# Performance work log

Hardware: AMD Instinct MI355X
Metric: run time of the kernel (lower is better)

## Reference

```python
import jax, jax.numpy as jnp
import numpy as np

RADIUS = 8
NUM_CORNERS = 500


def _dwconv(x, k2d, mode):
    # depthwise 2D conv on NCHW with explicit border padding (kornia-style)
    ph, pw = k2d.shape[0] // 2, k2d.shape[1] // 2
    xp = jnp.pad(x, ((0, 0), (0, 0), (ph, ph), (pw, pw)), mode=mode)
    C = x.shape[1]
    kern = jnp.broadcast_to(k2d[None, None], (C, 1, k2d.shape[0], k2d.shape[1])).astype(x.dtype)
    return jax.lax.conv_general_dilated(xp, kern, (1, 1), 'VALID',
                                        feature_group_count=C,
                                        dimension_numbers=('NCHW', 'OIHW', 'NCHW'))


def _gauss2d(k, sigma):
    x = jnp.arange(k, dtype=jnp.float32) - (k - 1) / 2.0
    g = jnp.exp(-(x * x) / (2.0 * sigma * sigma))
    g = g / g.sum()
    return jnp.outer(g, g)


def _nms2d(x):
    # kornia.feature.nms2d with (5,5) window: keep values equal to local max
    m = jax.lax.reduce_window(x, -jnp.inf, jax.lax.max, (1, 1, 5, 5), (1, 1, 1, 1), 'SAME')
    return x * (x == m).astype(x.dtype)


def _gftt(gray):
    # kornia CornerGFTT: sobel gradients (normalized /8, replicate pad),
    # structure tensor blurred with gaussian(7, sigma=1), min eigenvalue
    kx = jnp.array([[-1., 0., 1.], [-2., 0., 2.], [-1., 0., 1.]], jnp.float32) / 8.0
    dx = _dwconv(gray, kx, 'edge')
    dy = _dwconv(gray, kx.T, 'edge')
    g7 = _gauss2d(7, 1.0)
    dx2 = _dwconv(dx * dx, g7, 'reflect')
    dy2 = _dwconv(dy * dy, g7, 'reflect')
    dxy = _dwconv(dx * dy, g7, 'reflect')
    det = dx2 * dy2 - dxy * dxy
    tr = dx2 + dy2
    return 0.5 * (tr - jnp.sqrt(jnp.abs(tr * tr - 4.0 * det)))


def _laplacian5(x):
    # kornia laplacian kernel size 5, normalized by abs-sum (=48), reflect pad
    k = jnp.ones((5, 5), jnp.float32).at[2, 2].set(1.0 - 25.0)
    k = k / jnp.abs(k).sum()
    return _dwconv(x, k, 'reflect')


def _get_corners(imgs):
    B, _, H, W = imgs.shape
    r, N = RADIUS, NUM_CORNERS
    gray = 0.299 * imgs[:, :1] + 0.587 * imgs[:, 1:2] + 0.114 * imgs[:, 2:3]
    corners = _nms2d(_gftt(gray))
    # MaxPool2d(r, return_indices) + MaxUnpool2d(r): keep only per-block max
    blocks = corners.reshape(B, 1, H // r, r, W // r, r)
    bmax = blocks.max(axis=(3, 5), keepdims=True)
    unpooled = jnp.where(blocks == bmax, blocks, 0.0).reshape(B, 1, H, W)
    values, idx = jax.lax.top_k(unpooled.reshape(B, -1), N)   # [B,N]
    h, w = idx // W, idx % W
    b = jnp.repeat(jnp.arange(B), N)
    target = jnp.zeros((B, 1, H, W), imgs.dtype).at[b, 0, h.ravel(), w.ravel()].set(values.ravel())
    target = _nms2d(target)
    return (target > 0).astype(target.dtype)


def setup_inputs() -> dict:
    key = jax.random.key(0)
    k1, k2 = jax.random.split(key)
    scores_dense = jax.random.uniform(k1, (16, 1, 512, 512), dtype=jnp.float32)
    imgs = jax.random.uniform(k2, (16, 3, 512, 512), dtype=jnp.float32)
    return {"scores_dense": scores_dense, "imgs": imgs}


def reference(scores_dense, imgs):
    corners = _dwconv(_get_corners(imgs), _gauss2d(7, 1.0), 'reflect')
    lap = _laplacian5(scores_dense)
    logp = jnp.clip(jnp.log(scores_dense), -100.0)      # torch BCELoss clamps log at -100
    log1mp = jnp.clip(jnp.log1p(-scores_dense), -100.0)
    bce = -(corners * logp + (1.0 - corners) * log1mp).mean()
    return bce + (scores_dense * jnp.exp(-lap)).mean() * 10.0
```

## Files before the change

### kernel.cpp

```cpp
#include <hip/hip_runtime.h>
#include <math.h>

#define BB 16
#define HH 512
#define WW 512
#define HWP (HH*WW)
#define NPIX (BB*HWP)
#define HWP4 (HWP/4)
#define NG (NPIX/4)
#define NCORN 500
#define NSLOT 4096
#define OCAP 1024
#define NKEY (NSLOT+OCAP)
#define NKPT (NKEY/256)
#define NBL 2048
#define NPOSTB 320

__device__ __constant__ float G7c[7] = {
    0.0044330482f, 0.0540055826f, 0.2420362294f, 0.3990502793f,
    0.2420362294f, 0.0540055826f, 0.0044330482f};

__device__ __forceinline__ int reflect_idx(int i, int n) {
    if (i < 0) i = -i;
    if (i >= n) i = 2 * n - 2 - i;
    return i;
}

__device__ __forceinline__ float w1d(int p, int o, int n) {
    float w = 0.f;
    int d = p - o;
    if (d >= -3 && d <= 3) w += G7c[d + 3];
    if (p >= 1 && p + o <= 3) w += G7c[3 - p - o];
    if (p <= n - 2 && p + o >= 2 * n - 5) w += G7c[2 * n + 1 - p - o];
    return w;
}

__global__ void k_gray(const float* __restrict__ imgs, float* __restrict__ gray) {
    int g = blockIdx.x * blockDim.x + threadIdx.x;
    if (g >= NG) return;
    int b = g / HWP4, r = g % HWP4;
    const float4* base = (const float4*)(imgs + (size_t)b * 3 * HWP);
    float4 R = base[r], G = base[r + HWP4], Bc = base[r + 2 * HWP4];
    float4 o;
    o.x = 0.299f * R.x + 0.587f * G.x + 0.114f * Bc.x;
    o.y = 0.299f * R.y + 0.587f * G.y + 0.114f * Bc.y;
    o.z = 0.299f * R.z + 0.587f * G.z + 0.114f * Bc.z;
    o.w = 0.299f * R.w + 0.587f * G.w + 0.114f * Bc.w;
    ((float4*)gray)[g] = o;
}

__global__ __launch_bounds__(256) void k_front(const float* __restrict__ gray,
                                               float* __restrict__ S) {
    __shared__ float gt[24][72];
    __shared__ float pA[22][70], pC[22][70], pD[22][70];
    __shared__ float hA[22][64], hC[22][64], hD[22][64];
    int x0 = blockIdx.x * 64;
    int y0 = blockIdx.y * 16;
    int b = blockIdx.z;
    const float* gb = gray + (size_t)b * HWP;
    int tid = threadIdx.x;

    for (int idx = tid; idx < 24 * 72; idx += 256) {
        int r = idx / 72, c = idx % 72;
        int gy = min(max(y0 - 4 + r, 0), HH - 1);
        int gx = min(max(x0 - 4 + c, 0), WW - 1);
        gt[r][c] = gb[gy * WW + gx];
    }
    __syncthreads();

    for (int idx = tid; idx < 22 * 70; idx += 256) {
        int r = idx / 70, c = idx % 70;
        int py = y0 - 3 + r, px = x0 - 3 + c;
        if (py >= 0 && py < HH && px >= 0 && px < WW) {
            float g00 = gt[r][c],   g01 = gt[r][c+1],   g02 = gt[r][c+2];
            float g10 = gt[r+1][c],                     g12 = gt[r+1][c+2];
            float g20 = gt[r+2][c], g21 = gt[r+2][c+1], g22 = gt[r+2][c+2];
            float dx = (g02 - g00 + 2.f * (g12 - g10) + g22 - g20) * 0.125f;
            float dy = (g20 - g00 + 2.f * (g21 - g01) + g22 - g02) * 0.125f;
            pA[r][c] = dx * dx; pC[r][c] = dy * dy; pD[r][c] = dx * dy;
        }
    }
    __syncthreads();

    for (int idx = tid; idx < 22 * 64; idx += 256) {
        int r = idx / 64, c = idx % 64;
        int py = y0 - 3 + r;
        if (py >= 0 && py < HH) {
            int ox = x0 + c;
            float A = 0.f, C = 0.f, D = 0.f;
#pragma unroll
            for (int t = 0; t < 7; ++t) {
                int px = reflect_idx(ox - 3 + t, WW);
                int lc = px - (x0 - 3);
                float w = G7c[t];
                A += w * pA[r][lc]; C += w * pC[r][lc]; D += w * pD[r][lc];
            }
            hA[r][c] = A; hC[r][c] = C; hD[r][c] = D;
        }
    }
    __syncthreads();

    for (int idx = tid; idx < 16 * 64; idx += 256) {
        int r = idx / 64, c = idx % 64;
        int oy = y0 + r;
        float A = 0.f, C = 0.f, D = 0.f;
#pragma unroll
        for (int t = 0; t < 7; ++t) {
            int py = reflect_idx(oy - 3 + t, HH);
            int lr = py - (y0 - 3);
            float w = G7c[t];
            A += w * hA[lr][c]; C += w * hC[lr][c]; D += w * hD[lr][c];
        }
        float det = A * C - D * D;
        float tr = A + C;
        S[(size_t)b * HWP + (size_t)oy * WW + x0 + c] =
            0.5f * (tr - sqrtf(fabsf(tr * tr - 4.f * det)));
    }
}

__global__ void k_cand2(const float* __restrict__ S, float* __restrict__ sval,
                        int* __restrict__ sidx, int* __restrict__ ocnt) {
    __shared__ float tile[4][12][12];
    int wave = threadIdx.x >> 6, lane = threadIdx.x & 63;
    int tx = blockIdx.x * 4 + wave;
    int ty = blockIdx.y;
    int b = blockIdx.z;
    const float* sb = S + (size_t)b * HWP;
    for (int t = lane; t < 144; t += 64) {
        int r = t / 12, c = t % 12;
        int yy = min(max(ty * 8 - 2 + r, 0), HH - 1);
        int xx = min(max(tx * 8 - 2 + c, 0), WW - 1);
        tile[wave][r][c] = sb[yy * WW + xx];
    }
    __syncthreads();
    int ly = lane >> 3, lx = lane & 7;
    float v = tile[wave][ly + 2][lx + 2];
    float m = -INFINITY;
#pragma unroll
    for (int dy = 0; dy < 5; ++dy)
#pragma unroll
        for (int dx = 0; dx < 5; ++dx)
            m = fmaxf(m, tile[wave][ly + dy][lx + dx]);
    float cval = (v == m) ? v : 0.f;
    int y = ty * 8 + ly, x = tx * 8 + lx;
    float tm = cval;
#pragma unroll
    for (int off = 32; off; off >>= 1)
        tm = fmaxf(tm, __shfl_xor(tm, off));
    unsigned long long mask = __ballot(cval == tm && cval > 0.f);
    int slot = ty * 64 + tx;
    if (mask) {
        int first = __ffsll(mask) - 1;
        if (lane == first) {
            sval[b * NKEY + slot] = cval;
            sidx[b * NKEY + slot] = y * WW + x;
        } else if ((mask >> lane) & 1ull) {
            int pos = atomicAdd(&ocnt[b], 1);
            if (pos < OCAP) {
                sval[b * NKEY + NSLOT + pos] = cval;
                sidx[b * NKEY + NSLOT + pos] = y * WW + x;
            }
        }
    } else if (lane == 0) {
        sval[b * NKEY + slot] = 0.f;
        sidx[b * NKEY + slot] = 0;
    }
}

__global__ __launch_bounds__(256) void k_sel(const float* __restrict__ sval,
                       const int* __restrict__ sidx, const int* __restrict__ ocnt,
                       unsigned long long* __restrict__ selK) {
    __shared__ int shw[4];
    __shared__ int shtot;
    int b = blockIdx.x;
    int n = NSLOT + min(ocnt[b], OCAP);
    unsigned long long keys[NKPT];
    int cnt = 0;
#pragma unroll
    for (int t = 0; t < NKPT; ++t) {
        int i = threadIdx.x + t * 256;
        unsigned long long k = 0ull;
        if (i < n) {
            float v = sval[b * NKEY + i];
            if (v > 0.f) {
                unsigned int ix = (unsigned int)sidx[b * NKEY + i];
                k = ((unsigned long long)__float_as_uint(v) << 32) |
                    (unsigned long long)(~ix);
                cnt++;
            }
        }
        keys[t] = k;
    }
    int wid = threadIdx.x >> 6;
    {
        int c = cnt;
#pragma unroll
        for (int off = 32; off; off >>= 1) c += __shfl_down(c, off);
        if ((threadIdx.x & 63) == 0) shw[wid] = c;
        __syncthreads();
        if (threadIdx.x == 0) shtot = shw[0] + shw[1] + shw[2] + shw[3];
        __syncthreads();
    }
    int target = min(NCORN, shtot);
    unsigned long long T = 0ull;
    for (int bit = 63; bit >= 0; --bit) {
        unsigned long long cand = T | (1ull << bit);
        int c = 0;
#pragma unroll
        for (int t = 0; t < NKPT; ++t) c += (keys[t] >= cand) ? 1 : 0;
#pragma unroll
        for (int off = 32; off; off >>= 1) c += __shfl_down(c, off);
        __syncthreads();
        if ((threadIdx.x & 63) == 0) shw[wid] = c;
        __syncthreads();
        int tot = shw[0] + shw[1] + shw[2] + shw[3];
        if (tot >= target) T = cand;
    }
    if (threadIdx.x == 0) selK[b] = T;
}

__global__ __launch_bounds__(256) void k_post(const float* __restrict__ sval,
                       const int* __restrict__ sidx, const int* __restrict__ ocnt,
                       const unsigned long long* __restrict__ selK,
                       const float* __restrict__ scores,
                       float* __restrict__ partialC) {
    int gid = blockIdx.x * 256 + threadIdx.x;
    int b = gid / NKEY, s = gid - b * NKEY;
    int novf = min(ocnt[b], OCAP);
    float contrib = 0.f;
    float v = (s < NSLOT + novf) ? sval[gid] : 0.f;
    if (v > 0.f) {
        unsigned int ix = (unsigned int)sidx[gid];
        unsigned long long K = selK[b];
        unsigned long long k = ((unsigned long long)__float_as_uint(v) << 32) |
                               (unsigned long long)(~ix);
        if (k >= K) {
            int y = (int)(ix >> 9), x = (int)(ix & 511);
            const float* bsv = sval + b * NKEY;
            const int* bsi = sidx + b * NKEY;
            bool sup = false;
            int ty0 = max(y - 2, 0) >> 3, ty1 = min(y + 2, HH - 1) >> 3;
            int tx0 = max(x - 2, 0) >> 3, tx1 = min(x + 2, WW - 1) >> 3;
            for (int ty = ty0; ty <= ty1 && !sup; ++ty)
                for (int tx = tx0; tx <= tx1 && !sup; ++tx) {
                    int s2 = ty * 64 + tx;
                    float v2 = bsv[s2];
                    if (v2 <= v) continue;
                    int ix2 = bsi[s2];
                    unsigned long long k2 = ((unsigned long long)__float_as_uint(v2) << 32) |
                                            (unsigned long long)(~(unsigned int)ix2);
                    if (k2 < K) continue;
                    int y2 = ix2 >> 9, x2 = ix2 & 511;
                    if (abs(y2 - y) <= 2 && abs(x2 - x) <= 2) sup = true;
                }
            for (int j = 0; j < novf && !sup; ++j) {
                float v2 = bsv[NSLOT + j];
                if (v2 <= v) continue;
                int ix2 = bsi[NSLOT + j];
                unsigned long long k2 = ((unsigned long long)__float_as_uint(v2) << 32) |
                                        (unsigned long long)(~(unsigned int)ix2);
                if (k2 < K) continue;
                int y2 = ix2 >> 9, x2 = ix2 & 511;
                if (abs(y2 - y) <= 2 && abs(x2 - x) <= 2) sup = true;
            }
            if (!sup) {
                const float* sb = scores + (size_t)b * HWP;
                if (y >= 3 && y <= HH - 4 && x >= 3 && x <= WW - 4) {
#pragma unroll
                    for (int j = -3; j <= 3; ++j) {
                        float wy = G7c[j + 3];
#pragma unroll
                        for (int i = -3; i <= 3; ++i) {
                            float w = wy * G7c[i + 3];
                            float p = sb[(y + j) * WW + (x + i)];
                            float lp = fmaxf(__logf(p), -100.f);
                            float l1p = fmaxf(__logf(1.f - p), -100.f);
                            contrib += w * (lp - l1p);
                        }
                    }
                } else {
                    int oy0 = max(y - 6, 0), oy1 = min(y + 6, HH - 1);
                    int ox0 = max(x - 6, 0), ox1 = min(x + 6, WW - 1);
                    for (int oy = oy0; oy <= oy1; ++oy) {
                        float wy = w1d(y, oy, HH);
                        if (wy == 0.f) continue;
                        for (int ox = ox0; ox <= ox1; ++ox) {
                            float wx = w1d(x, ox, WW);
                            if (wx == 0.f) continue;
                            float p = sb[oy * WW + ox];
                            float lp = fmaxf(__logf(p), -100.f);
                            float l1p = fmaxf(__logf(1.f - p), -100.f);
                            contrib += wy * wx * (lp - l1p);
                        }
                    }
                }
            }
        }
    }
#pragma unroll
    for (int off = 32; off; off >>= 1) contrib += __shfl_down(contrib, off);
    __shared__ float wsum[4];
    int wid = threadIdx.x >> 6;
    if ((threadIdx.x & 63) == 0) wsum[wid] = contrib;
    __syncthreads();
    if (threadIdx.x == 0)
        partialC[blockIdx.x] = wsum[0] + wsum[1] + wsum[2] + wsum[3];
}

__global__ __launch_bounds__(256) void k_loss(const float* __restrict__ scores,
                                              float* __restrict__ partial) {
    __shared__ float st[8][520];
    __shared__ float h5[8][512];
    int b = blockIdx.x >> 7;
    int rg = blockIdx.x & 127;
    int y0 = rg * 4;
    const float* sb = scores + (size_t)b * HWP;
    int tid = threadIdx.x;
    for (int idx = tid; idx < 8 * 516; idx += 256) {
        int i = idx / 516, c = idx % 516;
        int gy = reflect_idx(y0 - 2 + i, HH);
        int gx = reflect_idx(c - 2, WW);
        st[i][c] = sb[gy * WW + gx];
    }
    __syncthreads();
    for (int idx = tid; idx < 8 * 512; idx += 256) {
        int i = idx >> 9, x = idx & 511;
        h5[i][x] = st[i][x] + st[i][x + 1] + st[i][x + 2] + st[i][x + 3] + st[i][x + 4];
    }
    __syncthreads();
    float a_loc = 0.f, b_loc = 0.f;
#pragma unroll
    for (int k = 0; k < 8; ++k) {
        int idx = tid + k * 256;
        int r = idx >> 9, x = idx & 511;
        float p = st[r + 2][x + 2];
        float s25 = h5[r][x] + h5[r + 1][x] + h5[r + 2][x] + h5[r + 3][x] + h5[r + 4][x];
        float l1p = fmaxf(__logf(1.f - p), -100.f);
        a_loc -= l1p;
        float lap = (s25 - 25.f * p) * (1.0f / 48.0f);
        b_loc += p * __expf(-lap);
    }
#pragma unroll
    for (int off = 32; off; off >>= 1) {
        a_loc += __shfl_down(a_loc, off);
        b_loc += __shfl_down(b_loc, off);
    }
    __shared__ float wa[4], wbs[4];
    int wid = threadIdx.x >> 6;
    if ((threadIdx.x & 63) == 0) { wa[wid] = a_loc; wbs[wid] = b_loc; }
    __syncthreads();
    if (threadIdx.x == 0) {
        partial[blockIdx.x] = wa[0] + wa[1] + wa[2] + wa[3];
        partial[NBL + blockIdx.x] = wbs[0] + wbs[1] + wbs[2] + wbs[3];
    }
}

__global__ void k_reduce(const float* __restrict__ partial, float* __restrict__ out) {
    float ta = 0.f, tb = 0.f, tc = 0.f;
    for (int i = threadIdx.x; i < NBL; i += blockDim.x) {
        ta += partial[i];
        tb += partial[NBL + i];
    }
    for (int i = threadIdx.x; i < NPOSTB; i += blockDim.x)
        tc += partial[2 * NBL + i];
#pragma unroll
    for (int off = 32; off; off >>= 1) {
        ta += __shfl_down(ta, off);
        tb += __shfl_down(tb, off);
        tc += __shfl_down(tc, off);
    }
    __shared__ float wa[4], wb[4], wc[4];
    int wid = threadIdx.x >> 6, lid = threadIdx.x & 63;
    if (lid == 0) { wa[wid] = ta; wb[wid] = tb; wc[wid] = tc; }
    __syncthreads();
    if (threadIdx.x == 0) {
        float A = wa[0] + wa[1] + wa[2] + wa[3];
        float Bv = wb[0] + wb[1] + wb[2] + wb[3];
        float C = wc[0] + wc[1] + wc[2] + wc[3];
        float invN = 1.0f / (float)NPIX;
        out[0] = (A - C) * invN + 10.0f * Bv * invN;
    }
}

extern "C" void kernel_launch(void* const* d_in, const int* in_sizes, int n_in,
                              void* d_out, int out_size, void* d_ws, size_t ws_size,
                              hipStream_t stream) {
    const float* scores = (const float*)d_in[0];
    const float* imgs   = (const float*)d_in[1];
    float* out = (float*)d_out;

    float* ws = (float*)d_ws;
    float* A0 = ws;
    float* A1 = ws + (size_t)NPIX;
    float* sval = ws + 2 * (size_t)NPIX;
    int*   sidx = (int*)(sval + (size_t)BB * NKEY);
    int*   ocnt = (int*)(sidx + (size_t)BB * NKEY);
    unsigned long long* selK = (unsigned long long*)(ocnt + BB);
    float* partial = (float*)(selK + BB);

    const int T = 256;
    const int GG = NG / T;

    k_gray <<<GG, T, 0, stream>>>(imgs, A0);
    k_front<<<dim3(8, 32, BB), T, 0, stream>>>(A0, A1);

    hipMemsetAsync(ocnt, 0, BB * sizeof(int), stream);
    dim3 gcand(16, 64, BB);
    k_cand2<<<gcand, 256, 0, stream>>>(A1, sval, sidx, ocnt);

    k_sel<<<BB, 256, 0, stream>>>(sval, sidx, ocnt, selK);
    k_post<<<NPOSTB, 256, 0, stream>>>(sval, sidx, ocnt, selK, scores,
                                       partial + 2 * NBL);
    k_loss<<<NBL, T, 0, stream>>>(scores, partial);
    k_reduce<<<1, 256, 0, stream>>>(partial, out);
}
```

Baseline: 266.6 us.

## Fuse grayscale into front kernel, merge select/post, fold reduction into loss

Grayscale conversion moves into the structure-tensor kernel, so the separate gray image is no longer written and re-read. The front kernel reuses one shared buffer, uses row-structured indexing and takes a fast path without reflect-index math for interior tiles. The top-k select and post-processing kernels merge into one per-batch kernel that keeps keys in registers, and the final reduction becomes a last-block-done step inside the loss kernel. This removes several launches and intermediate round trips, but the post work now runs on only 16 blocks instead of 320, which lowers parallelism for that stage.

```diff
diff --git a/kernel.cpp b/kernel.cpp
--- a/kernel.cpp
+++ b/kernel.cpp
@@ -6,15 +6,21 @@
 #define WW 512
 #define HWP (HH*WW)
 #define NPIX (BB*HWP)
-#define HWP4 (HWP/4)
-#define NG (NPIX/4)
 #define NCORN 500
 #define NSLOT 4096
 #define OCAP 1024
 #define NKEY (NSLOT+OCAP)
 #define NKPT (NKEY/256)
 #define NBL 2048
-#define NPOSTB 320
+
+#define GT  0
+#define PAo 1728
+#define PCo 3268
+#define PDo 4808
+#define HAo 0
+#define HCo 6348
+#define HDo 7756
+#define FBUF 9164
 
 __device__ __constant__ float G7c[7] = {
     0.0044330482f, 0.0540055826f, 0.2420362294f, 0.3990502793f,
@@ -35,102 +41,125 @@
     return w;
 }
 
-__global__ void k_gray(const float* __restrict__ imgs, float* __restrict__ gray) {
-    int g = blockIdx.x * blockDim.x + threadIdx.x;
-    if (g >= NG) return;
-    int b = g / HWP4, r = g % HWP4;
-    const float4* base = (const float4*)(imgs + (size_t)b * 3 * HWP);
-    float4 R = base[r], G = base[r + HWP4], Bc = base[r + 2 * HWP4];
-    float4 o;
-    o.x = 0.299f * R.x + 0.587f * G.x + 0.114f * Bc.x;
-    o.y = 0.299f * R.y + 0.587f * G.y + 0.114f * Bc.y;
-    o.z = 0.299f * R.z + 0.587f * G.z + 0.114f * Bc.z;
-    o.w = 0.299f * R.w + 0.587f * G.w + 0.114f * Bc.w;
-    ((float4*)gray)[g] = o;
-}
-
-__global__ __launch_bounds__(256) void k_front(const float* __restrict__ gray,
+__global__ __launch_bounds__(256) void k_front(const float* __restrict__ imgs,
                                                float* __restrict__ S) {
-    __shared__ float gt[24][72];
-    __shared__ float pA[22][70], pC[22][70], pD[22][70];
-    __shared__ float hA[22][64], hC[22][64], hD[22][64];
-    int x0 = blockIdx.x * 64;
-    int y0 = blockIdx.y * 16;
-    int b = blockIdx.z;
-    const float* gb = gray + (size_t)b * HWP;
+    __shared__ float B[FBUF];
+    int x0 = blockIdx.x * 64, y0 = blockIdx.y * 16, b = blockIdx.z;
+    const float* ib = imgs + (size_t)b * 3 * HWP;
     int tid = threadIdx.x;
-
-    for (int idx = tid; idx < 24 * 72; idx += 256) {
-        int r = idx / 72, c = idx % 72;
-        int gy = min(max(y0 - 4 + r, 0), HH - 1);
-        int gx = min(max(x0 - 4 + c, 0), WW - 1);
-        gt[r][c] = gb[gy * WW + gx];
-    }
-    __syncthreads();
-
-    for (int idx = tid; idx < 22 * 70; idx += 256) {
-        int r = idx / 70, c = idx % 70;
-        int py = y0 - 3 + r, px = x0 - 3 + c;
-        if (py >= 0 && py < HH && px >= 0 && px < WW) {
-            float g00 = gt[r][c],   g01 = gt[r][c+1],   g02 = gt[r][c+2];
-            float g10 = gt[r+1][c],                     g12 = gt[r+1][c+2];
-            float g20 = gt[r+2][c], g21 = gt[r+2][c+1], g22 = gt[r+2][c+2];
+    int r0 = tid >> 6, c0 = tid & 63;
+
+    for (int rr = r0; rr < 24; rr += 4) {
+        int gy = min(max(y0 - 4 + rr, 0), HH - 1);
+        const float* rowp = ib + (size_t)gy * WW;
+        {
+            int gx = min(max(x0 - 4 + c0, 0), WW - 1);
+            float R = rowp[gx], G = rowp[HWP + gx], Bl = rowp[2 * HWP + gx];
+            B[GT + rr * 72 + c0] = 0.299f * R + 0.587f * G + 0.114f * Bl;
+        }
+        if (c0 < 8) {
+            int c = c0 + 64;
+            int gx = min(max(x0 - 4 + c, 0), WW - 1);
+            float R = rowp[gx], G = rowp[HWP + gx], Bl = rowp[2 * HWP + gx];
+            B[GT + rr * 72 + c] = 0.299f * R + 0.587f * G + 0.114f * Bl;
+        }
+    }
+    __syncthreads();
+
+    for (int rr = r0; rr < 22; rr += 4) {
+#pragma unroll
+        for (int half = 0; half < 2; ++half) {
+            int cc = c0 + half * 64;
+            if (half == 1 && c0 >= 6) break;
+            int base = GT + rr * 72 + cc;
+            float g00 = B[base],       g01 = B[base + 1],   g02 = B[base + 2];
+            float g10 = B[base + 72],                        g12 = B[base + 74];
+            float g20 = B[base + 144], g21 = B[base + 145], g22 = B[base + 146];
             float dx = (g02 - g00 + 2.f * (g12 - g10) + g22 - g20) * 0.125f;
             float dy = (g20 - g00 + 2.f * (g21 - g01) + g22 - g02) * 0.125f;
-            pA[r][c] = dx * dx; pC[r][c] = dy * dy; pD[r][c] = dx * dy;
-        }
-    }
-    __syncthreads();
-
-    for (int idx = tid; idx < 22 * 64; idx += 256) {
-        int r = idx / 64, c = idx % 64;
-        int py = y0 - 3 + r;
-        if (py >= 0 && py < HH) {
-            int ox = x0 + c;
-            float A = 0.f, C = 0.f, D = 0.f;
+            int po = rr * 70 + cc;
+            B[PAo + po] = dx * dx;
+            B[PCo + po] = dy * dy;
+            B[PDo + po] = dx * dy;
+        }
+    }
+    __syncthreads();
+
+    bool ex = (x0 == 0) || (x0 == WW - 64);
+    for (int rr = r0; rr < 22; rr += 4) {
+        float A = 0.f, C = 0.f, D = 0.f;
+        if (!ex) {
+            int base = rr * 70 + c0;
 #pragma unroll
             for (int t = 0; t < 7; ++t) {
-                int px = reflect_idx(ox - 3 + t, WW);
-                int lc = px - (x0 - 3);
                 float w = G7c[t];
-                A += w * pA[r][lc]; C += w * pC[r][lc]; D += w * pD[r][lc];
-            }
-            hA[r][c] = A; hC[r][c] = C; hD[r][c] = D;
-        }
-    }
-    __syncthreads();
-
-    for (int idx = tid; idx < 16 * 64; idx += 256) {
-        int r = idx / 64, c = idx % 64;
-        int oy = y0 + r;
+                A += w * B[PAo + base + t];
+                C += w * B[PCo + base + t];
+                D += w * B[PDo + base + t];
+            }
+        } else {
+#pragma unroll
+            for (int t = 0; t < 7; ++t) {
+                int px = reflect_idx(x0 + c0 - 3 + t, WW);
+                int lc = rr * 70 + (px - (x0 - 3));
+                float w = G7c[t];
+                A += w * B[PAo + lc];
+                C += w * B[PCo + lc];
+                D += w * B[PDo + lc];
+            }
+        }
+        int ho = rr * 64 + c0;
+        B[HAo + ho] = A; B[HCo + ho] = C; B[HDo + ho] = D;
+    }
+    __syncthreads();
+
+    bool ey = (y0 == 0) || (y0 == HH - 16);
+    for (int rr = r0; rr < 16; rr += 4) {
         float A = 0.f, C = 0.f, D = 0.f;
-#pragma unroll
-        for (int t = 0; t < 7; ++t) {
-            int py = reflect_idx(oy - 3 + t, HH);
-            int lr = py - (y0 - 3);
-            float w = G7c[t];
-            A += w * hA[lr][c]; C += w * hC[lr][c]; D += w * hD[lr][c];
+        if (!ey) {
+#pragma unroll
+            for (int t = 0; t < 7; ++t) {
+                int lo = (rr + t) * 64 + c0;
+                float w = G7c[t];
+                A += w * B[HAo + lo];
+                C += w * B[HCo + lo];
+                D += w * B[HDo + lo];
+            }
+        } else {
+#pragma unroll
+            for (int t = 0; t < 7; ++t) {
+                int py = reflect_idx(y0 + rr - 3 + t, HH);
+                int lo = (py - (y0 - 3)) * 64 + c0;
+                float w = G7c[t];
+                A += w * B[HAo + lo];
+                C += w * B[HCo + lo];
+                D += w * B[HDo + lo];
+            }
         }
         float det = A * C - D * D;
         float tr = A + C;
-        S[(size_t)b * HWP + (size_t)oy * WW + x0 + c] =
+        S[(size_t)b * HWP + (size_t)(y0 + rr) * WW + x0 + c0] =
             0.5f * (tr - sqrtf(fabsf(tr * tr - 4.f * det)));
     }
 }
 
 __global__ void k_cand2(const float* __restrict__ S, float* __restrict__ sval,
                         int* __restrict__ sidx, int* __restrict__ ocnt) {
-    __shared__ float tile[4][12][12];
+    __shared__ float tile[4][12][16];
     int wave = threadIdx.x >> 6, lane = threadIdx.x & 63;
     int tx = blockIdx.x * 4 + wave;
     int ty = blockIdx.y;
     int b = blockIdx.z;
     const float* sb = S + (size_t)b * HWP;
-    for (int t = lane; t < 144; t += 64) {
-        int r = t / 12, c = t % 12;
-        int yy = min(max(ty * 8 - 2 + r, 0), HH - 1);
-        int xx = min(max(tx * 8 - 2 + c, 0), WW - 1);
-        tile[wave][r][c] = sb[yy * WW + xx];
+#pragma unroll
+    for (int t = 0; t < 3; ++t) {
+        int e = lane + t * 64;
+        int r = e >> 4, c = e & 15;
+        if (c < 12) {
+            int yy = min(max(ty * 8 - 2 + r, 0), HH - 1);
+            int xx = min(max(tx * 8 - 2 + c, 0), WW - 1);
+            tile[wave][r][c] = sb[yy * WW + xx];
+        }
     }
     __syncthreads();
     int ly = lane >> 3, lx = lane & 7;
@@ -167,13 +196,15 @@
     }
 }
 
-__global__ __launch_bounds__(256) void k_sel(const float* __restrict__ sval,
+__global__ __launch_bounds__(256) void k_selpost(const float* __restrict__ sval,
                        const int* __restrict__ sidx, const int* __restrict__ ocnt,
-                       unsigned long long* __restrict__ selK) {
+                       const float* __restrict__ scores,
+                       float* __restrict__ partialC) {
     __shared__ int shw[4];
     __shared__ int shtot;
     int b = blockIdx.x;
-    int n = NSLOT + min(ocnt[b], OCAP);
+    int novf = min(ocnt[b], OCAP);
+    int n = NSLOT + novf;
     unsigned long long keys[NKPT];
     int cnt = 0;
 #pragma unroll
@@ -202,9 +233,9 @@
         __syncthreads();
     }
     int target = min(NCORN, shtot);
-    unsigned long long T = 0ull;
+    unsigned long long K = 0ull;
     for (int bit = 63; bit >= 0; --bit) {
-        unsigned long long cand = T | (1ull << bit);
+        unsigned long long cand = K | (1ull << bit);
         int c = 0;
 #pragma unroll
         for (int t = 0; t < NKPT; ++t) c += (keys[t] >= cand) ? 1 : 0;
@@ -214,30 +245,19 @@
         if ((threadIdx.x & 63) == 0) shw[wid] = c;
         __syncthreads();
         int tot = shw[0] + shw[1] + shw[2] + shw[3];
-        if (tot >= target) T = cand;
-    }
-    if (threadIdx.x == 0) selK[b] = T;
-}
-
-__global__ __launch_bounds__(256) void k_post(const float* __restrict__ sval,
-                       const int* __restrict__ sidx, const int* __restrict__ ocnt,
-                       const unsigned long long* __restrict__ selK,
-                       const float* __restrict__ scores,
-                       float* __restrict__ partialC) {
-    int gid = blockIdx.x * 256 + threadIdx.x;
-    int b = gid / NKEY, s = gid - b * NKEY;
-    int novf = min(ocnt[b], OCAP);
+        if (tot >= target) K = cand;
+    }
+    const float* bsv = sval + b * NKEY;
+    const int* bsi = sidx + b * NKEY;
+    const float* sb = scores + (size_t)b * HWP;
     float contrib = 0.f;
-    float v = (s < NSLOT + novf) ? sval[gid] : 0.f;
-    if (v > 0.f) {
-        unsigned int ix = (unsigned int)sidx[gid];
-        unsigned long long K = selK[b];
-        unsigned long long k = ((unsigned long long)__float_as_uint(v) << 32) |
-                               (unsigned long long)(~ix);
-        if (k >= K) {
+#pragma unroll
+    for (int t = 0; t < NKPT; ++t) {
+        unsigned long long k = keys[t];
+        if (k != 0ull && k >= K && target > 0) {
+            unsigned int ix = ~(unsigned int)(k & 0xffffffffull);
+            float v = __uint_as_float((unsigned int)(k >> 32));
             int y = (int)(ix >> 9), x = (int)(ix & 511);
-            const float* bsv = sval + b * NKEY;
-            const int* bsi = sidx + b * NKEY;
             bool sup = false;
             int ty0 = max(y - 2, 0) >> 3, ty1 = min(y + 2, HH - 1) >> 3;
             int tx0 = max(x - 2, 0) >> 3, tx1 = min(x + 2, WW - 1) >> 3;
@@ -264,7 +284,6 @@
                 if (abs(y2 - y) <= 2 && abs(x2 - x) <= 2) sup = true;
             }
             if (!sup) {
-                const float* sb = scores + (size_t)b * HWP;
                 if (y >= 3 && y <= HH - 4 && x >= 3 && x <= WW - 4) {
 #pragma unroll
                     for (int j = -3; j <= 3; ++j) {
@@ -300,30 +319,42 @@
 #pragma unroll
     for (int off = 32; off; off >>= 1) contrib += __shfl_down(contrib, off);
     __shared__ float wsum[4];
-    int wid = threadIdx.x >> 6;
     if ((threadIdx.x & 63) == 0) wsum[wid] = contrib;
     __syncthreads();
     if (threadIdx.x == 0)
-        partialC[blockIdx.x] = wsum[0] + wsum[1] + wsum[2] + wsum[3];
+        partialC[b] = wsum[0] + wsum[1] + wsum[2] + wsum[3];
 }
 
 __global__ __launch_bounds__(256) void k_loss(const float* __restrict__ scores,
-                                              float* __restrict__ partial) {
+                                              float* __restrict__ partial,
+                                              int* __restrict__ lcnt,
+                                              float* __restrict__ out) {
     __shared__ float st[8][520];
     __shared__ float h5[8][512];
-    int b = blockIdx.x >> 7;
-    int rg = blockIdx.x & 127;
-    int y0 = rg * 4;
+    int bid = blockIdx.x;
+    int b = bid >> 7;
+    int y0 = (bid & 127) * 4;
     const float* sb = scores + (size_t)b * HWP;
     int tid = threadIdx.x;
-    for (int idx = tid; idx < 8 * 516; idx += 256) {
-        int i = idx / 516, c = idx % 516;
-        int gy = reflect_idx(y0 - 2 + i, HH);
-        int gx = reflect_idx(c - 2, WW);
-        st[i][c] = sb[gy * WW + gx];
-    }
-    __syncthreads();
-    for (int idx = tid; idx < 8 * 512; idx += 256) {
+    int r0 = tid >> 6, c0 = tid & 63;
+    for (int rr = r0; rr < 8; rr += 4) {
+        int gy = reflect_idx(y0 - 2 + rr, HH);
+        const float* src = sb + (size_t)gy * WW;
+#pragma unroll
+        for (int j = 0; j < 9; ++j) {
+            int c = c0 + j * 64;
+            if (c < 516) {
+                int gx = c - 2;
+                gx = (gx < 0) ? -gx : gx;
+                gx = (gx > WW - 1) ? 2 * WW - 2 - gx : gx;
+                st[rr][c] = src[gx];
+            }
+        }
+    }
+    __syncthreads();
+#pragma unroll
+    for (int k = 0; k < 16; ++k) {
+        int idx = tid + k * 256;
         int i = idx >> 9, x = idx & 511;
         h5[i][x] = st[i][x] + st[i][x + 1] + st[i][x + 2] + st[i][x + 3] + st[i][x + 4];
     }
@@ -337,8 +368,7 @@
         float s25 = h5[r][x] + h5[r + 1][x] + h5[r + 2][x] + h5[r + 3][x] + h5[r + 4][x];
         float l1p = fmaxf(__logf(1.f - p), -100.f);
         a_loc -= l1p;
-        float lap = (s25 - 25.f * p) * (1.0f / 48.0f);
-        b_loc += p * __expf(-lap);
+        b_loc += p * __expf((25.f * p - s25) * (1.0f / 48.0f));
     }
 #pragma unroll
     for (int off = 32; off; off >>= 1) {
@@ -346,39 +376,42 @@
         b_loc += __shfl_down(b_loc, off);
     }
     __shared__ float wa[4], wbs[4];
-    int wid = threadIdx.x >> 6;
-    if ((threadIdx.x & 63) == 0) { wa[wid] = a_loc; wbs[wid] = b_loc; }
-    __syncthreads();
-    if (threadIdx.x == 0) {
-        partial[blockIdx.x] = wa[0] + wa[1] + wa[2] + wa[3];
-        partial[NBL + blockIdx.x] = wbs[0] + wbs[1] + wbs[2] + wbs[3];
-    }
-}
-
-__global__ void k_reduce(const float* __restrict__ partial, float* __restrict__ out) {
-    float ta = 0.f, tb = 0.f, tc = 0.f;
-    for (int i = threadIdx.x; i < NBL; i += blockDim.x) {
-        ta += partial[i];
-        tb += partial[NBL + i];
-    }
-    for (int i = threadIdx.x; i < NPOSTB; i += blockDim.x)
-        tc += partial[2 * NBL + i];
-#pragma unroll
-    for (int off = 32; off; off >>= 1) {
-        ta += __shfl_down(ta, off);
-        tb += __shfl_down(tb, off);
-        tc += __shfl_down(tc, off);
-    }
-    __shared__ float wa[4], wb[4], wc[4];
-    int wid = threadIdx.x >> 6, lid = threadIdx.x & 63;
-    if (lid == 0) { wa[wid] = ta; wb[wid] = tb; wc[wid] = tc; }
-    __syncthreads();
-    if (threadIdx.x == 0) {
-        float A = wa[0] + wa[1] + wa[2] + wa[3];
-        float Bv = wb[0] + wb[1] + wb[2] + wb[3];
-        float C = wc[0] + wc[1] + wc[2] + wc[3];
-        float invN = 1.0f / (float)NPIX;
-        out[0] = (A - C) * invN + 10.0f * Bv * invN;
+    __shared__ bool islast;
+    int wid = tid >> 6;
+    if ((tid & 63) == 0) { wa[wid] = a_loc; wbs[wid] = b_loc; }
+    __syncthreads();
+    if (tid == 0) {
+        partial[bid] = wa[0] + wa[1] + wa[2] + wa[3];
+        partial[NBL + bid] = wbs[0] + wbs[1] + wbs[2] + wbs[3];
+        __threadfence();
+        int old = atomicAdd(lcnt, 1);
+        islast = (old == NBL - 1);
+    }
+    __syncthreads();
+    if (islast) {
+        __threadfence();
+        float ta = 0.f, tb = 0.f, tc = 0.f;
+        for (int i = tid; i < NBL; i += 256) {
+            ta += partial[i];
+            tb += partial[NBL + i];
+        }
+        if (tid < BB) tc = partial[2 * NBL + tid];
+#pragma unroll
+        for (int off = 32; off; off >>= 1) {
+            ta += __shfl_down(ta, off);
+            tb += __shfl_down(tb, off);
+            tc += __shfl_down(tc, off);
+        }
+        __shared__ float fa[4], fb[4], fc[4];
+        if ((tid & 63) == 0) { fa[wid] = ta; fb[wid] = tb; fc[wid] = tc; }
+        __syncthreads();
+        if (tid == 0) {
+            float A = fa[0] + fa[1] + fa[2] + fa[3];
+            float Bv = fb[0] + fb[1] + fb[2] + fb[3];
+            float C = fc[0] + fc[1] + fc[2] + fc[3];
+            float invN = 1.0f / (float)NPIX;
+            out[0] = (A - C) * invN + 10.0f * Bv * invN;
+        }
     }
 }
 
@@ -390,27 +423,21 @@
     float* out = (float*)d_out;
 
     float* ws = (float*)d_ws;
-    float* A0 = ws;
-    float* A1 = ws + (size_t)NPIX;
-    float* sval = ws + 2 * (size_t)NPIX;
+    float* S = ws;
+    float* sval = ws + (size_t)NPIX;
     int*   sidx = (int*)(sval + (size_t)BB * NKEY);
     int*   ocnt = (int*)(sidx + (size_t)BB * NKEY);
-    unsigned long long* selK = (unsigned long long*)(ocnt + BB);
-    float* partial = (float*)(selK + BB);
-
-    const int T = 256;
-    const int GG = NG / T;
-
-    k_gray <<<GG, T, 0, stream>>>(imgs, A0);
-    k_front<<<dim3(8, 32, BB), T, 0, stream>>>(A0, A1);
-
-    hipMemsetAsync(ocnt, 0, BB * sizeof(int), stream);
+    int*   lcnt = ocnt + BB;
+    float* partial = (float*)(lcnt + 1);
+
+    hipMemsetAsync(ocnt, 0, (BB + 1) * sizeof(int), stream);
+
+    k_front<<<dim3(8, 32, BB), 256, 0, stream>>>(imgs, S);
+
     dim3 gcand(16, 64, BB);
-    k_cand2<<<gcand, 256, 0, stream>>>(A1, sval, sidx, ocnt);
-
-    k_sel<<<BB, 256, 0, stream>>>(sval, sidx, ocnt, selK);
-    k_post<<<NPOSTB, 256, 0, stream>>>(sval, sidx, ocnt, selK, scores,
-                                       partial + 2 * NBL);
-    k_loss<<<NBL, T, 0, stream>>>(scores, partial);
-    k_reduce<<<1, 256, 0, stream>>>(partial, out);
-}
+    k_cand2<<<gcand, 256, 0, stream>>>(S, sval, sidx, ocnt);
+
+    k_selpost<<<BB, 256, 0, stream>>>(sval, sidx, ocnt, scores, partial + 2 * NBL);
+
+    k_loss<<<NBL, 256, 0, stream>>>(scores, partial, lcnt, out);
+}
```

Measured after the change: 537.3 us. 2.02x slower.
